# Performance work log

Hardware: AMD Instinct MI355X
Metric: run time of the kernel (lower is better)

## Reference

```python
import jax, jax.numpy as jnp
import numpy as np

N_HEAD = 12
N_EMBD = 768
HEAD_DIM = N_EMBD // N_HEAD
B, S = 4, 2048


def setup_inputs() -> dict:
    key = jax.random.key(0)
    k1, k2, k3, k4, k5 = jax.random.split(key, 5)
    x = jax.random.normal(k1, (B, S, N_EMBD), dtype=jnp.float32)
    # causal additive mask: 1.0 where attention is disallowed (strictly upper triangle)
    mask = (1.0 - jnp.tril(jnp.ones((S, S), dtype=jnp.float32)))[None, None, :, :]
    scale = 0.02
    W_attn = jax.random.normal(k2, (N_EMBD, 3 * N_EMBD), dtype=jnp.float32) * scale
    b_attn = jnp.zeros((3 * N_EMBD,), dtype=jnp.float32)
    W_proj = jax.random.normal(k3, (N_EMBD, N_EMBD), dtype=jnp.float32) * scale
    b_proj = jnp.zeros((N_EMBD,), dtype=jnp.float32)
    return {"x": x, "mask": mask, "W_attn": W_attn, "b_attn": b_attn,
            "W_proj": W_proj, "b_proj": b_proj}


def reference(x, mask, W_attn, b_attn, W_proj, b_proj):
    Bn, Sn, _ = x.shape
    qkv = x @ W_attn + b_attn                      # [B,S,3E]
    q, k, v = jnp.split(qkv, 3, axis=-1)           # each [B,S,E]

    def heads(t):
        return t.reshape(Bn, Sn, N_HEAD, HEAD_DIM).transpose(0, 2, 1, 3)  # [B,H,S,D]

    q, k, v = heads(q), heads(k), heads(v)
    attn = jnp.einsum('bhqd,bhkd->bhqk', q, k) / jnp.sqrt(jnp.float32(HEAD_DIM))
    attn = attn + mask * (-1e9)
    attn = jax.nn.softmax(attn, axis=-1)
    # dropout in inference mode = identity
    out = jnp.einsum('bhqk,bhkd->bhqd', attn, v)   # [B,H,S,D]
    out = out.transpose(0, 2, 1, 3).reshape(Bn, Sn, N_EMBD)
    return out @ W_proj + b_proj
```

## Files before the change

### kernel.cpp

```cpp
#include <hip/hip_runtime.h>
#include <stdint.h>

#define NHEAD 12
#define HDIM  64
#define EMB   768
#define N3    2304
#define SEQ   2048
#define BATCH 4
#define MROWS 8192

#define QSCALE 0.18033688011112042f

typedef __bf16 bf16_t;
typedef __bf16 bf16x8 __attribute__((ext_vector_type(8)));
typedef __bf16 bf16x4 __attribute__((ext_vector_type(4)));
typedef short  s16x4  __attribute__((ext_vector_type(4)));
typedef float  f32x4  __attribute__((ext_vector_type(4)));

__device__ __forceinline__ void gld_lds16(void* lds, const void* g) {
    __builtin_amdgcn_global_load_lds((const __attribute__((address_space(1))) void*)g,
                                     (__attribute__((address_space(3))) void*)lds,
                                     16, 0, 0);
}

__device__ __forceinline__ float fast_exp2(float x) {
    return __builtin_amdgcn_exp2f(x);
}

__device__ __forceinline__ f32x4 mfma16_bf16(bf16x4 a, bf16x4 b, f32x4 c) {
#if __has_builtin(__builtin_amdgcn_mfma_f32_16x16x16_bf16)
    return __builtin_amdgcn_mfma_f32_16x16x16_bf16(a, b, c, 0, 0, 0);
#else
    union U { bf16x4 h; s16x4 s; };
    U ua, ub; ua.h = a; ub.h = b;
    return __builtin_amdgcn_mfma_f32_16x16x16bf16_1k(ua.s, ub.s, c, 0, 0, 0);
#endif
}

__global__ __launch_bounds__(256) void cvt_x_k(const float* __restrict__ x,
                                               bf16_t* __restrict__ xb, int n8) {
    int idx    = blockIdx.x * blockDim.x + threadIdx.x;
    int stride = gridDim.x * blockDim.x;
    for (int i = idx; i < n8; i += stride) {
        float4 a = ((const float4*)x)[i * 2];
        float4 b = ((const float4*)x)[i * 2 + 1];
        bf16x8 v;
        v[0] = (bf16_t)a.x; v[1] = (bf16_t)a.y; v[2] = (bf16_t)a.z; v[3] = (bf16_t)a.w;
        v[4] = (bf16_t)b.x; v[5] = (bf16_t)b.y; v[6] = (bf16_t)b.z; v[7] = (bf16_t)b.w;
        ((bf16x8*)xb)[i] = v;
    }
}

__global__ __launch_bounds__(256) void transpose_cvt_k(
    const float* __restrict__ W, bf16_t* __restrict__ WT, int K, int N) {
    __shared__ float tile[32][33];
    const int n0 = blockIdx.x * 32, k0 = blockIdx.y * 32;
    const int tx = threadIdx.x & 31, ty = threadIdx.x >> 5;
#pragma unroll
    for (int i = 0; i < 32; i += 8)
        tile[ty + i][tx] = W[(size_t)(k0 + ty + i) * N + (n0 + tx)];
    __syncthreads();
#pragma unroll
    for (int i = 0; i < 32; i += 8)
        WT[(size_t)(n0 + ty + i) * K + (k0 + tx)] = (bf16_t)tile[tx][ty + i];
}

template<int MODE>
__global__ __launch_bounds__(256) void gemm_kernel(
    const bf16_t* __restrict__ Av,
    const bf16_t* __restrict__ BT,
    const float* __restrict__ bias,
    float* __restrict__ out,
    bf16_t* __restrict__ qbuf,
    bf16_t* __restrict__ kbuf,
    bf16_t* __restrict__ vbuf,
    int Ncols)
{
    const int K = 768;
    __shared__ alignas(16) bf16_t As[2][128 * 32];
    __shared__ alignas(16) bf16_t Bs[2][128 * 32];

    const int tid    = threadIdx.x;
    const int wave   = tid >> 6;
    const int lane   = tid & 63;
    const int lane15 = lane & 15;
    const int quad   = lane >> 4;

    const int bid   = blockIdx.x;
    const int chunk = (int)(gridDim.x >> 3);
    const int swz   = (bid & 7) * chunk + (bid >> 3);
    const int NB    = Ncols >> 7;
    const int mBase = (swz / NB) * 128;
    const int nBase = (swz % NB) * 128;

    const int wm = (wave >> 1) * 64;
    const int wn = (wave & 1) * 64;

    f32x4 acc[4][4];
#pragma unroll
    for (int i = 0; i < 4; i++)
#pragma unroll
        for (int j = 0; j < 4; j++) acc[i][j] = (f32x4){0.f, 0.f, 0.f, 0.f};

    const bf16_t* aSrc = Av + (size_t)mBase * K;
    const bf16_t* bSrc = BT + (size_t)nBase * K;

    const int srow = lane >> 2;
    const int sch  = lane & 3;

    auto issueA = [&](int k0, int buf) {
#pragma unroll
        for (int p = 0; p < 2; p++) {
            int r0  = p * 64 + wave * 16;
            int row = r0 + srow;
            int lch = sch ^ (row & 3);
            gld_lds16(&As[buf][r0 * 32], aSrc + (size_t)row * K + k0 + lch * 8);
        }
    };
    auto issueB = [&](int k0, int buf) {
#pragma unroll
        for (int p = 0; p < 2; p++) {
            int r0  = p * 64 + wave * 16;
            int row = r0 + srow;
            int lch = sch ^ (row & 3);
            gld_lds16(&Bs[buf][r0 * 32], bSrc + (size_t)row * K + k0 + lch * 8);
        }
    };

    issueA(0, 0);
    issueB(0, 0);

    for (int k0 = 0, it = 0; k0 < K; k0 += 32, it++) {
        const int buf = it & 1;
        __syncthreads();
        if (k0 + 32 < K) {
            issueB(k0 + 32, buf ^ 1);
            issueA(k0 + 32, buf ^ 1);
        }

        bf16x8 aF[4], bF[4];
#pragma unroll
        for (int t = 0; t < 4; t++) {
            int ra = wm + t * 16 + lane15;
            int rb = wn + t * 16 + lane15;
            aF[t] = *(const bf16x8*)&As[buf][ra * 32 + (quad ^ (ra & 3)) * 8];
            bF[t] = *(const bf16x8*)&Bs[buf][rb * 32 + (quad ^ (rb & 3)) * 8];
        }
#pragma unroll
        for (int i = 0; i < 4; i++)
#pragma unroll
            for (int j = 0; j < 4; j++)
                acc[i][j] = __builtin_amdgcn_mfma_f32_16x16x32_bf16(aF[i], bF[j], acc[i][j], 0, 0, 0);
    }

    const int region = nBase / EMB;
#pragma unroll
    for (int i = 0; i < 4; i++) {
#pragma unroll
        for (int j = 0; j < 4; j++) {
            int gn = nBase + wn + j * 16 + lane15;
            float bv = bias[gn];
            if (region == 2) {
                int within = gn - 2 * EMB;
                int h = within >> 6, d = within & 63;
                int gm0 = mBase + wm + i * 16 + quad * 4;
                int b = gm0 >> 11, s = gm0 & 2047;
                int bh = b * NHEAD + h;
                bf16x4 v4;
#pragma unroll
                for (int r = 0; r < 4; r++) v4[r] = (bf16_t)(acc[i][j][r] + bv);
                *(bf16x4*)&vbuf[((size_t)bh * HDIM + d) * SEQ + s] = v4;
            } else {
                bf16_t* dst = (region == 0) ? qbuf : kbuf;
                const float scale = (region == 0) ? QSCALE : 1.0f;
                int within = gn - region * EMB;
                int h = within >> 6, d = within & 63;
#pragma unroll
                for (int r = 0; r < 4; r++) {
                    int gm = mBase + wm + i * 16 + quad * 4 + r;
                    int b = gm >> 11, s = gm & 2047;
                    int bh = b * NHEAD + h;
                    dst[((size_t)bh * SEQ + s) * HDIM + d] = (bf16_t)((acc[i][j][r] + bv) * scale);
                }
            }
        }
    }
}

__global__ __launch_bounds__(256) void proj_kernel(
    const bf16_t* __restrict__ Av,
    const bf16_t* __restrict__ BT,
    const float*  __restrict__ bias,
    float* __restrict__ out)
{
    const int K = 768;
    __shared__ alignas(16) bf16_t As[2][64 * 32];
    __shared__ alignas(16) bf16_t Bs[2][128 * 32];

    const int tid    = threadIdx.x;
    const int wave   = tid >> 6;
    const int lane   = tid & 63;
    const int lane15 = lane & 15;
    const int quad   = lane >> 4;

    const int bid   = blockIdx.x;
    const int swz   = (bid & 7) * 96 + (bid >> 3);
    const int mBase = (swz / 6) * 64;
    const int nBase = (swz % 6) * 128;

    f32x4 acc[4][2];
#pragma unroll
    for (int t = 0; t < 4; t++)
#pragma unroll
        for (int u = 0; u < 2; u++) acc[t][u] = (f32x4){0.f, 0.f, 0.f, 0.f};

    const bf16_t* aSrc = Av + (size_t)mBase * K;
    const bf16_t* bSrc = BT + (size_t)nBase * K;

    const int srow = lane >> 2;
    const int sch  = lane & 3;

    auto issueA = [&](int k0, int buf) {
        int r0  = wave * 16;
        int row = r0 + srow;
        int lch = sch ^ (row & 3);
        gld_lds16(&As[buf][r0 * 32], aSrc + (size_t)row * K + k0 + lch * 8);
    };
    auto issueB = [&](int k0, int buf) {
#pragma unroll
        for (int p = 0; p < 2; p++) {
            int r0  = p * 64 + wave * 16;
            int row = r0 + srow;
            int lch = sch ^ (row & 3);
            gld_lds16(&Bs[buf][r0 * 32], bSrc + (size_t)row * K + k0 + lch * 8);
        }
    };

    issueA(0, 0);
    issueB(0, 0);

    for (int k0 = 0, it = 0; k0 < K; k0 += 32, it++) {
        const int buf = it & 1;
        __syncthreads();
        if (k0 + 32 < K) {
            issueB(k0 + 32, buf ^ 1);
            issueA(k0 + 32, buf ^ 1);
        }

        bf16x8 aF[4], bF[2];
#pragma unroll
        for (int t = 0; t < 4; t++) {
            int ra = t * 16 + lane15;
            aF[t] = *(const bf16x8*)&As[buf][ra * 32 + (quad ^ (ra & 3)) * 8];
        }
#pragma unroll
        for (int u = 0; u < 2; u++) {
            int rb = wave * 32 + u * 16 + lane15;
            bF[u] = *(const bf16x8*)&Bs[buf][rb * 32 + (quad ^ (rb & 3)) * 8];
        }
#pragma unroll
        for (int t = 0; t < 4; t++)
#pragma unroll
            for (int u = 0; u < 2; u++)
                acc[t][u] = __builtin_amdgcn_mfma_f32_16x16x32_bf16(aF[t], bF[u], acc[t][u], 0, 0, 0);
    }

#pragma unroll
    for (int t = 0; t < 4; t++) {
#pragma unroll
        for (int u = 0; u < 2; u++) {
            int gn = nBase + wave * 32 + u * 16 + lane15;
            float bv = bias[gn];
#pragma unroll
            for (int r = 0; r < 4; r++) {
                int gm = mBase + t * 16 + quad * 4 + r;
                out[(size_t)gm * EMB + gn] = acc[t][u][r] + bv;
            }
        }
    }
}

__global__ __launch_bounds__(256) void attn_kernel(
    const bf16_t* __restrict__ qbuf,
    const bf16_t* __restrict__ kbuf,
    const bf16_t* __restrict__ vtbuf,
    bf16_t* __restrict__ obuf)
{
    __shared__ alignas(16) bf16_t Ks[2][64 * 64];
    __shared__ alignas(16) bf16_t Vs[2][64 * 64];
    __shared__ alignas(16) bf16_t Plds[4][16 * 72];

    const int tid    = threadIdx.x;
    const int wave   = tid >> 6;
    const int lane   = tid & 63;
    const int lane15 = lane & 15;
    const int quad   = lane >> 4;

    const int bid = blockIdx.x;
    const int swz = (bid & 7) * 96 + (bid >> 3);
    const int bh = swz >> 4;
    const int j  = swz & 15;

    const bf16_t* Qp = qbuf  + (size_t)bh * SEQ * HDIM;
    const bf16_t* Kp = kbuf  + (size_t)bh * SEQ * HDIM;
    const bf16_t* Vp = vtbuf + (size_t)bh * HDIM * SEQ;
    bf16_t* pl = &Plds[wave][0];
    const int b = bh / NHEAD, h = bh % NHEAD;

    const int srow8 = lane >> 3;
    const int sch8  = lane & 7;

    auto issueKV = [&](int kb, int buf) {
#pragma unroll
        for (int p = 0; p < 2; p++) {
            int r0  = p * 32 + wave * 8;
            int row = r0 + srow8;
            int lch = sch8 ^ (row & 7);
            gld_lds16(&Ks[buf][r0 * 64], Kp + (size_t)(kb + row) * HDIM + lch * 8);
            gld_lds16(&Vs[buf][r0 * 64], Vp + (size_t)row * SEQ + kb + lch * 8);
        }
    };

    for (int seg = 0; seg < 2; seg++) {
        const int qt = seg ? (31 - j) : j;
        const int q0 = qt * 64 + wave * 16;

        const bf16x8 qf0 = *(const bf16x8*)&Qp[(size_t)(q0 + lane15) * HDIM + quad * 8];
        const bf16x8 qf1 = *(const bf16x8*)&Qp[(size_t)(q0 + lane15) * HDIM + 32 + quad * 8];

        float lrow = 0.f;
        f32x4 oT[4];
#pragma unroll
        for (int t = 0; t < 4; t++) oT[t] = (f32x4){0.f, 0.f, 0.f, 0.f};

        const int nT = qt + 1;
        __syncthreads();
        issueKV(0, 0);

        for (int kt = 0; kt < nT; kt++) {
            const int buf = kt & 1;
            __syncthreads();
            if (kt + 1 < nT) issueKV((kt + 1) * 64, buf ^ 1);

            const int kb = kt * 64;

            f32x4 sT[4];
            __builtin_amdgcn_s_setprio(1);
#pragma unroll
            for (int kg = 0; kg < 4; kg++) {
                sT[kg] = (f32x4){0.f, 0.f, 0.f, 0.f};
                int row = kg * 16 + lane15;
                bf16x8 kf0 = *(const bf16x8*)&Ks[buf][row * 64 + ((quad    ) ^ (row & 7)) * 8];
                bf16x8 kf1 = *(const bf16x8*)&Ks[buf][row * 64 + ((quad + 4) ^ (row & 7)) * 8];
                sT[kg] = __builtin_amdgcn_mfma_f32_16x16x32_bf16(kf0, qf0, sT[kg], 0, 0, 0);
                sT[kg] = __builtin_amdgcn_mfma_f32_16x16x32_bf16(kf1, qf1, sT[kg], 0, 0, 0);
            }
            __builtin_amdgcn_s_setprio(0);

            if (kb + 64 > q0) {
                const int query = q0 + lane15;
#pragma unroll
                for (int kg = 0; kg < 4; kg++) {
                    int key0 = kb + kg * 16 + quad * 4;
#pragma unroll
                    for (int r = 0; r < 4; r++)
                        sT[kg][r] = (key0 + r <= query) ? sT[kg][r] : -1e30f;
                }
            }

            bf16x4 pf[4];
#pragma unroll
            for (int kg = 0; kg < 4; kg++) {
#pragma unroll
                for (int r = 0; r < 4; r++) sT[kg][r] = fast_exp2(sT[kg][r]);
                lrow += (sT[kg][0] + sT[kg][1]) + (sT[kg][2] + sT[kg][3]);
                bf16x4 v;
#pragma unroll
                for (int r = 0; r < 4; r++) v[r] = (bf16_t)sT[kg][r];
                pf[kg] = v;
            }

            __builtin_amdgcn_s_setprio(1);
#pragma unroll
            for (int t = 0; t < 4; t++) {
                int vrow = t * 16 + lane15;
#pragma unroll
                for (int kg = 0; kg < 4; kg++) {
                    int c    = kg * 2 + (quad >> 1);
                    int phys = c ^ (vrow & 7);
                    bf16x4 vf = *(const bf16x4*)&Vs[buf][vrow * 64 + phys * 8 + (quad & 1) * 4];
                    oT[t] = mfma16_bf16(vf, pf[kg], oT[t]);
                }
            }
            __builtin_amdgcn_s_setprio(0);
        }

        lrow += __shfl_xor(lrow, 16, 64);
        lrow += __shfl_xor(lrow, 32, 64);
        const float inv = 1.0f / lrow;

#pragma unroll
        for (int t = 0; t < 4; t++)
#pragma unroll
            for (int r = 0; r < 4; r++)
                pl[lane15 * 72 + t * 16 + quad * 4 + r] = (bf16_t)(oT[t][r] * inv);

        const int qrow = lane >> 2;
        const int ch   = lane & 3;
        bf16_t* orow = &obuf[((size_t)(b * SEQ + q0 + qrow)) * EMB + h * HDIM];
#pragma unroll
        for (int p = 0; p < 2; p++) {
            bf16x8 v = *(const bf16x8*)&pl[qrow * 72 + (ch + p * 4) * 8];
            *(bf16x8*)&orow[(ch + p * 4) * 8] = v;
        }
    }
}

extern "C" void kernel_launch(void* const* d_in, const int* in_sizes, int n_in,
                              void* d_out, int out_size, void* d_ws, size_t ws_size,
                              hipStream_t stream) {
    const float* x      = (const float*)d_in[0];
    const float* W_attn = (const float*)d_in[2];
    const float* b_attn = (const float*)d_in[3];
    const float* W_proj = (const float*)d_in[4];
    const float* b_proj = (const float*)d_in[5];
    float* out = (float*)d_out;

    bf16_t* ws  = (bf16_t*)d_ws;
    bf16_t* WaT = ws;
    bf16_t* WpT = WaT + (size_t)N3 * EMB;
    bf16_t* Qb  = WpT + (size_t)EMB * EMB;
    bf16_t* Kb  = Qb + (size_t)BATCH * NHEAD * SEQ * HDIM;
    bf16_t* Vt  = Kb + (size_t)BATCH * NHEAD * SEQ * HDIM;
    bf16_t* Ob  = Vt + (size_t)BATCH * NHEAD * SEQ * HDIM;
    bf16_t* xb  = Ob;

    transpose_cvt_k<<<dim3(N3 / 32, EMB / 32), 256, 0, stream>>>(W_attn, WaT, EMB, N3);
    transpose_cvt_k<<<dim3(EMB / 32, EMB / 32), 256, 0, stream>>>(W_proj, WpT, EMB, EMB);
    cvt_x_k<<<1536, 256, 0, stream>>>(x, xb, MROWS * EMB / 8);

    gemm_kernel<1><<<1152, 256, 0, stream>>>(
        xb, WaT, b_attn, nullptr, Qb, Kb, Vt, N3);

    attn_kernel<<<BATCH * NHEAD * 16, 256, 0, stream>>>(Qb, Kb, Vt, Ob);

    proj_kernel<<<768, 256, 0, stream>>>(Ob, WpT, b_proj, out);
}
```

Measured before the change: 223.9 us.

## Fuse prep kernels into one launch and double proj GEMM K-tile

Merges the two weight transpose/convert kernels and the x conversion kernel into one prep kernel, dispatched by block index, to cut two launches. Separately, the output projection GEMM now stages K-tiles of 64 instead of 32, with an 8-chunk XOR swizzle. That halves the number of barrier and prefetch iterations at the cost of twice the LDS per block, which may lower occupancy.

After: 218.1 us. 2.6% less time.

```diff
diff --git a/kernel.cpp b/kernel.cpp
--- a/kernel.cpp
+++ b/kernel.cpp
@@ -37,32 +37,40 @@
 #endif
 }
 
-__global__ __launch_bounds__(256) void cvt_x_k(const float* __restrict__ x,
-                                               bf16_t* __restrict__ xb, int n8) {
-    int idx    = blockIdx.x * blockDim.x + threadIdx.x;
-    int stride = gridDim.x * blockDim.x;
-    for (int i = idx; i < n8; i += stride) {
-        float4 a = ((const float4*)x)[i * 2];
-        float4 b = ((const float4*)x)[i * 2 + 1];
-        bf16x8 v;
-        v[0] = (bf16_t)a.x; v[1] = (bf16_t)a.y; v[2] = (bf16_t)a.z; v[3] = (bf16_t)a.w;
-        v[4] = (bf16_t)b.x; v[5] = (bf16_t)b.y; v[6] = (bf16_t)b.z; v[7] = (bf16_t)b.w;
-        ((bf16x8*)xb)[i] = v;
-    }
-}
-
-__global__ __launch_bounds__(256) void transpose_cvt_k(
-    const float* __restrict__ W, bf16_t* __restrict__ WT, int K, int N) {
+__global__ __launch_bounds__(256) void prep_kernel(
+    const float* __restrict__ Wa, bf16_t* __restrict__ WaT,
+    const float* __restrict__ Wp, bf16_t* __restrict__ WpT,
+    const float* __restrict__ x,  bf16_t* __restrict__ xb)
+{
     __shared__ float tile[32][33];
-    const int n0 = blockIdx.x * 32, k0 = blockIdx.y * 32;
-    const int tx = threadIdx.x & 31, ty = threadIdx.x >> 5;
-#pragma unroll
-    for (int i = 0; i < 32; i += 8)
-        tile[ty + i][tx] = W[(size_t)(k0 + ty + i) * N + (n0 + tx)];
-    __syncthreads();
-#pragma unroll
-    for (int i = 0; i < 32; i += 8)
-        WT[(size_t)(n0 + ty + i) * K + (k0 + tx)] = (bf16_t)tile[tx][ty + i];
+    const int bid = blockIdx.x;
+    if (bid < 2304) {
+        const float* W; bf16_t* WT; int K, N, b;
+        if (bid < 1728) { W = Wa; WT = WaT; K = 768; N = 2304; b = bid; }
+        else            { W = Wp; WT = WpT; K = 768; N = 768;  b = bid - 1728; }
+        const int nb = N / 32;
+        const int n0 = (b % nb) * 32, k0 = (b / nb) * 32;
+        const int tx = threadIdx.x & 31, ty = threadIdx.x >> 5;
+#pragma unroll
+        for (int i = 0; i < 32; i += 8)
+            tile[ty + i][tx] = W[(size_t)(k0 + ty + i) * N + (n0 + tx)];
+        __syncthreads();
+#pragma unroll
+        for (int i = 0; i < 32; i += 8)
+            WT[(size_t)(n0 + ty + i) * K + (k0 + tx)] = (bf16_t)tile[tx][ty + i];
+    } else {
+        const int n8 = MROWS * EMB / 8;
+        int idx    = (bid - 2304) * 256 + threadIdx.x;
+        const int stride = 1536 * 256;
+        for (int i = idx; i < n8; i += stride) {
+            float4 a = ((const float4*)x)[i * 2];
+            float4 b = ((const float4*)x)[i * 2 + 1];
+            bf16x8 v;
+            v[0] = (bf16_t)a.x; v[1] = (bf16_t)a.y; v[2] = (bf16_t)a.z; v[3] = (bf16_t)a.w;
+            v[4] = (bf16_t)b.x; v[5] = (bf16_t)b.y; v[6] = (bf16_t)b.z; v[7] = (bf16_t)b.w;
+            ((bf16x8*)xb)[i] = v;
+        }
+    }
 }
 
 template<int MODE>
@@ -194,8 +202,8 @@
     float* __restrict__ out)
 {
     const int K = 768;
-    __shared__ alignas(16) bf16_t As[2][64 * 32];
-    __shared__ alignas(16) bf16_t Bs[2][128 * 32];
+    __shared__ alignas(16) bf16_t As[2][64 * 64];
+    __shared__ alignas(16) bf16_t Bs[2][128 * 64];
 
     const int tid    = threadIdx.x;
     const int wave   = tid >> 6;
@@ -217,52 +225,60 @@
     const bf16_t* aSrc = Av + (size_t)mBase * K;
     const bf16_t* bSrc = BT + (size_t)nBase * K;
 
-    const int srow = lane >> 2;
-    const int sch  = lane & 3;
+    const int srow8 = lane >> 3;
+    const int sch8  = lane & 7;
 
     auto issueA = [&](int k0, int buf) {
-        int r0  = wave * 16;
-        int row = r0 + srow;
-        int lch = sch ^ (row & 3);
-        gld_lds16(&As[buf][r0 * 32], aSrc + (size_t)row * K + k0 + lch * 8);
+#pragma unroll
+        for (int p = 0; p < 2; p++) {
+            int r0  = wave * 8 + p * 32;
+            int row = r0 + srow8;
+            int lch = sch8 ^ (row & 7);
+            gld_lds16(&As[buf][r0 * 64], aSrc + (size_t)row * K + k0 + lch * 8);
+        }
     };
     auto issueB = [&](int k0, int buf) {
 #pragma unroll
-        for (int p = 0; p < 2; p++) {
-            int r0  = p * 64 + wave * 16;
-            int row = r0 + srow;
-            int lch = sch ^ (row & 3);
-            gld_lds16(&Bs[buf][r0 * 32], bSrc + (size_t)row * K + k0 + lch * 8);
+        for (int p = 0; p < 4; p++) {
+            int r0  = wave * 8 + p * 32;
+            int row = r0 + srow8;
+            int lch = sch8 ^ (row & 7);
+            gld_lds16(&Bs[buf][r0 * 64], bSrc + (size_t)row * K + k0 + lch * 8);
         }
     };
 
     issueA(0, 0);
     issueB(0, 0);
 
-    for (int k0 = 0, it = 0; k0 < K; k0 += 32, it++) {
+    for (int k0 = 0, it = 0; k0 < K; k0 += 64, it++) {
         const int buf = it & 1;
         __syncthreads();
-        if (k0 + 32 < K) {
-            issueB(k0 + 32, buf ^ 1);
-            issueA(k0 + 32, buf ^ 1);
-        }
-
-        bf16x8 aF[4], bF[2];
-#pragma unroll
-        for (int t = 0; t < 4; t++) {
-            int ra = t * 16 + lane15;
-            aF[t] = *(const bf16x8*)&As[buf][ra * 32 + (quad ^ (ra & 3)) * 8];
-        }
-#pragma unroll
-        for (int u = 0; u < 2; u++) {
-            int rb = wave * 32 + u * 16 + lane15;
-            bF[u] = *(const bf16x8*)&Bs[buf][rb * 32 + (quad ^ (rb & 3)) * 8];
-        }
-#pragma unroll
-        for (int t = 0; t < 4; t++)
-#pragma unroll
-            for (int u = 0; u < 2; u++)
-                acc[t][u] = __builtin_amdgcn_mfma_f32_16x16x32_bf16(aF[t], bF[u], acc[t][u], 0, 0, 0);
+        if (k0 + 64 < K) {
+            issueB(k0 + 64, buf ^ 1);
+            issueA(k0 + 64, buf ^ 1);
+        }
+
+        bf16x8 aF[2][4], bF[2][2];
+#pragma unroll
+        for (int kk = 0; kk < 2; kk++) {
+#pragma unroll
+            for (int t = 0; t < 4; t++) {
+                int ra = t * 16 + lane15;
+                aF[kk][t] = *(const bf16x8*)&As[buf][ra * 64 + (((quad + kk * 4) ^ (ra & 7)) * 8)];
+            }
+#pragma unroll
+            for (int u = 0; u < 2; u++) {
+                int rb = wave * 32 + u * 16 + lane15;
+                bF[kk][u] = *(const bf16x8*)&Bs[buf][rb * 64 + (((quad + kk * 4) ^ (rb & 7)) * 8)];
+            }
+        }
+#pragma unroll
+        for (int kk = 0; kk < 2; kk++)
+#pragma unroll
+            for (int t = 0; t < 4; t++)
+#pragma unroll
+                for (int u = 0; u < 2; u++)
+                    acc[t][u] = __builtin_amdgcn_mfma_f32_16x16x32_bf16(aF[kk][t], bF[kk][u], acc[t][u], 0, 0, 0);
     }
 
 #pragma unroll
@@ -435,9 +451,7 @@
     bf16_t* Ob  = Vt + (size_t)BATCH * NHEAD * SEQ * HDIM;
     bf16_t* xb  = Ob;
 
-    transpose_cvt_k<<<dim3(N3 / 32, EMB / 32), 256, 0, stream>>>(W_attn, WaT, EMB, N3);
-    transpose_cvt_k<<<dim3(EMB / 32, EMB / 32), 256, 0, stream>>>(W_proj, WpT, EMB, EMB);
-    cvt_x_k<<<1536, 256, 0, stream>>>(x, xb, MROWS * EMB / 8);
+    prep_kernel<<<3840, 256, 0, stream>>>(W_attn, WaT, W_proj, WpT, x, xb);
 
     gemm_kernel<1><<<1152, 256, 0, stream>>>(
         xb, WaT, b_attn, nullptr, Qb, Kb, Vt, N3);
```
